# Optimization experiments

Measured on AMD Instinct MI355X. Metric: run time of the kernel, lower is better.

## Reference

```python
import jax, jax.numpy as jnp
import numpy as np

N_NODES = 100000
N_EDGES = 1600000
F_IN = 128
N_HEADS = 4
F_OUT = 32
NEG_SLOPE = 0.2


def setup_inputs() -> dict:
    key = jax.random.key(0)
    k_feat, k_src, k_dst, k_w, k_as, k_ad, k_res = jax.random.split(key, 7)
    feat = jax.random.normal(k_feat, (N_NODES, F_IN), dtype=jnp.float32)
    src = jax.random.randint(k_src, (N_EDGES,), 0, N_NODES, dtype=jnp.int32)
    dst = jax.random.randint(k_dst, (N_EDGES,), 0, N_NODES, dtype=jnp.int32)
    s = 1.0 / np.sqrt(F_IN)
    W = jax.random.normal(k_w, (F_IN, N_HEADS * F_OUT), dtype=jnp.float32) * s
    att_src = jax.random.normal(k_as, (N_HEADS, F_OUT), dtype=jnp.float32) * 0.1
    att_dst = jax.random.normal(k_ad, (N_HEADS, F_OUT), dtype=jnp.float32) * 0.1
    W_res = jax.random.normal(k_res, (F_IN, N_HEADS * F_OUT), dtype=jnp.float32) * s
    return {"feat": feat, "W": W, "att_src": att_src, "att_dst": att_dst,
            "W_res": W_res, "src": src, "dst": dst}


def reference(feat, W, att_src, att_dst, W_res, src, dst):
    N = feat.shape[0]
    H, Fo = att_src.shape
    # shared linear projection (GATConv, bias=False): [N, H, Fo]
    x = (feat @ W).reshape(N, H, Fo)
    # per-node attention logits: [N, H]
    a_s = jnp.einsum('nhf,hf->nh', x, att_src)
    a_d = jnp.einsum('nhf,hf->nh', x, att_dst)
    # edge-wise scores + LeakyReLU: [E, H]
    e = jax.nn.leaky_relu(a_s[src] + a_d[dst], negative_slope=NEG_SLOPE)
    # segment softmax over incoming edges of each dst node
    e_max = jax.ops.segment_max(e, dst, num_segments=N)  # [N, H]
    e_exp = jnp.exp(e - e_max[dst])                       # [E, H]
    denom = jax.ops.segment_sum(e_exp, dst, num_segments=N)  # [N, H]
    alpha = e_exp / denom[dst]                            # [E, H]
    # weighted scatter-add aggregation: [N, H, Fo]
    msg = x[src] * alpha[:, :, None]
    out = jax.ops.segment_sum(msg, dst, num_segments=N)
    # residual projection
    res = (feat @ W_res).reshape(N, H, Fo)
    return out + res
```

## Files before the change

### kernel.cpp

```cpp
#include <hip/hip_runtime.h>
#include <math.h>

#define NN 100000
#define NE 1600000
#define F_IN 128
#define C 128
#define NEG_SLOPE 0.2f
#define PROJ_NB ((NN + 63) / 64)

#define NBLK1 256
#define EPB ((NE + NBLK1 - 1) / NBLK1)
#define BSHIFT 9
#define NBUCK ((NN + 511) / 512)

#define WCONV_NB 16
#define FAT1_NB (WCONV_NB + NBLK1)
#define FAT2_NB (NBLK1 + PROJ_NB)

typedef __attribute__((ext_vector_type(8))) short short8;
typedef __attribute__((ext_vector_type(4))) float f32x4;
typedef __attribute__((ext_vector_type(4))) float floatx4;
typedef __attribute__((ext_vector_type(4))) unsigned short ushortx4;

static __device__ __forceinline__ unsigned short f2bf(float f) {
    unsigned int u = __float_as_uint(f);
    unsigned int r = (u + 0x7fff + ((u >> 16) & 1)) >> 16;
    return (unsigned short)r;
}
static __device__ __forceinline__ float bf2f(unsigned short h) {
    return __uint_as_float((unsigned int)h << 16);
}
static __device__ __forceinline__ float lrelu(float x) {
    return (x > 0.f) ? x : NEG_SLOPE * x;
}

__global__ __launch_bounds__(256)
void fat1_kernel(const float* __restrict__ W,
                 const float* __restrict__ Wr,
                 unsigned short* __restrict__ Btf,
                 const int* __restrict__ dst,
                 int* __restrict__ counts)
{
    __shared__ int h[256];
    const int tid = threadIdx.x;

    if (blockIdx.x < WCONV_NB) {
        int g = blockIdx.x * 256 + tid;
        int nt = g >> 8;
        int kc = (g >> 6) & 3;
        int l  = g & 63;
        int n  = nt * 16 + (l & 15);
        int kb = kc * 32 + (l >> 4) * 8;
        unsigned short v[8];
        #pragma unroll
        for (int j = 0; j < 8; ++j) {
            int k = kb + j;
            float f = (n < 128) ? W[(size_t)k * 128 + n]
                                : Wr[(size_t)k * 128 + (n - 128)];
            v[j] = f2bf(f);
        }
        *(short8*)&Btf[(size_t)g * 8] = *(short8*)v;
        return;
    }

    const int hb = blockIdx.x - WCONV_NB;
    h[tid] = 0;
    __syncthreads();
    const int e0 = hb * EPB;
    const int e1 = min(NE, e0 + EPB);
    for (int e = e0 + tid; e < e1; e += 256)
        atomicAdd(&h[dst[e] >> BSHIFT], 1);
    __syncthreads();
    counts[tid * NBLK1 + hb] = h[tid];
}

__global__ __launch_bounds__(256)
void sortscan_kernel(int* __restrict__ counts, int* __restrict__ bucket_base)
{
    __shared__ int wsum[4];
    const int t = threadIdx.x, lane = t & 63, wid = t >> 6;
    const int base = t * NBLK1;
    int run = 0;
    #pragma unroll 8
    for (int g = 0; g < NBLK1 / 4; ++g) {
        int4 c = *(const int4*)&counts[base + g * 4];
        int4 w;
        w.x = run;
        w.y = w.x + c.x;
        w.z = w.y + c.y;
        w.w = w.z + c.z;
        run = w.w + c.w;
        *(int4*)&counts[base + g * 4] = w;
    }
    int v0 = run, v = run;
    #pragma unroll
    for (int off = 1; off < 64; off <<= 1) {
        int u = __shfl_up(v, off, 64);
        if (lane >= off) v += u;
    }
    if (lane == 63) wsum[wid] = v;
    __syncthreads();
    if (t == 0) {
        int r = 0;
        #pragma unroll
        for (int s = 0; s < 4; ++s) { int tmp = wsum[s]; wsum[s] = r; r += tmp; }
    }
    __syncthreads();
    int excl = wsum[wid] + (v - v0);
    bucket_base[t] = excl;
    if (t == 255) bucket_base[256] = excl + v0;
}

__global__ __launch_bounds__(256, 4)
void fat2_kernel(const int* __restrict__ src, const int* __restrict__ dst,
                 const int* __restrict__ counts,
                 const int* __restrict__ bucket_base,
                 int* __restrict__ bpack,
                 const float* __restrict__ feat,
                 const unsigned short* __restrict__ Btf,
                 const float* __restrict__ att_src,
                 const float* __restrict__ att_dst,
                 unsigned short* __restrict__ xb,
                 unsigned short* __restrict__ resb,
                 float* __restrict__ a_s,
                 float* __restrict__ a_d)
{
    __shared__ __align__(16) char smem[19456];
    const int tid = threadIdx.x;

    if (blockIdx.x < NBLK1) {
        int* cur = (int*)smem;
        cur[tid] = bucket_base[tid] + counts[tid * NBLK1 + blockIdx.x];
        __syncthreads();
        const int e0 = blockIdx.x * EPB;
        const int e1 = min(NE, e0 + EPB);
        for (int e = e0 + tid; e < e1; e += 256) {
            int d = dst[e];
            int s = src[e];
            int pos = atomicAdd(&cur[d >> BSHIFT], 1);
            bpack[pos] = ((d & 511) << 20) | s;
        }
        return;
    }

    const int pb = blockIdx.x - NBLK1;
    float* T2base = (float*)smem;
    float (*s_as)[4] = (float(*)[4])(smem + 17408);
    float (*s_ad)[4] = (float(*)[4])(smem + 18432);

    const int base = pb * 64;
    const int l = tid & 63;
    const int w = tid >> 6;
    const int quad = l >> 4;
    const int lo16 = l & 15;
    const int arow = w * 16 + lo16;
    const int nclamp = min(base + arow, NN - 1);

    short8 af[4];
    #pragma unroll
    for (int kc = 0; kc < 4; ++kc) {
        const float* fp = &feat[(size_t)nclamp * F_IN + kc * 32 + quad * 8];
        floatx4 f0 = __builtin_nontemporal_load((const floatx4*)fp);
        floatx4 f1 = __builtin_nontemporal_load((const floatx4*)(fp + 4));
        unsigned short v[8];
        v[0] = f2bf(f0.x); v[1] = f2bf(f0.y); v[2] = f2bf(f0.z); v[3] = f2bf(f0.w);
        v[4] = f2bf(f1.x); v[5] = f2bf(f1.y); v[6] = f2bf(f1.z); v[7] = f2bf(f1.w);
        af[kc] = *(short8*)v;
    }

    f32x4 acc[16];
    #pragma unroll
    for (int nt = 0; nt < 16; ++nt) acc[nt] = (f32x4){0.f, 0.f, 0.f, 0.f};

    #pragma unroll
    for (int nt = 0; nt < 16; ++nt) {
        const unsigned short* bp = &Btf[(size_t)(nt * 4) * 512 + l * 8];
        short8 b0 = *(const short8*)&bp[0];
        short8 b1 = *(const short8*)&bp[512];
        short8 b2 = *(const short8*)&bp[1024];
        short8 b3 = *(const short8*)&bp[1536];
        acc[nt] = __builtin_amdgcn_mfma_f32_16x16x32_bf16(af[0], b0, acc[nt], 0, 0, 0);
        acc[nt] = __builtin_amdgcn_mfma_f32_16x16x32_bf16(af[1], b1, acc[nt], 0, 0, 0);
        acc[nt] = __builtin_amdgcn_mfma_f32_16x16x32_bf16(af[2], b2, acc[nt], 0, 0, 0);
        acc[nt] = __builtin_amdgcn_mfma_f32_16x16x32_bf16(af[3], b3, acc[nt], 0, 0, 0);
    }

    float* T2 = T2base + w * (16 * 68);
    const int g  = l >> 4;
    const int cf = (l & 15) * 4;

    #pragma unroll
    for (int p = 0; p < 2; ++p) {
        #pragma unroll
        for (int ntl = 0; ntl < 4; ++ntl) {
            int nt = p * 4 + ntl;
            #pragma unroll
            for (int r = 0; r < 4; ++r)
                T2[(quad * 4 + r) * 68 + ntl * 16 + lo16] = acc[nt][r];
        }
        floatx4 ws4 = *(const floatx4*)&att_src[p * 64 + cf];
        floatx4 wd4 = *(const floatx4*)&att_dst[p * 64 + cf];
        float ps[4], pd[4];
        #pragma unroll
        for (int it = 0; it < 4; ++it) {
            int row = it * 4 + g;
            floatx4 v = *(floatx4*)&T2[row * 68 + cf];
            int node = base + w * 16 + row;
            ushortx4 hh;
            hh.x = f2bf(v.x); hh.y = f2bf(v.y); hh.z = f2bf(v.z); hh.w = f2bf(v.w);
            if (node < NN)
                __builtin_nontemporal_store(hh,
                    (ushortx4*)&xb[(size_t)node * C + p * 64 + cf]);
            ps[it] = v.x * ws4.x + v.y * ws4.y + v.z * ws4.z + v.w * ws4.w;
            pd[it] = v.x * wd4.x + v.y * wd4.y + v.z * wd4.z + v.w * wd4.w;
        }
        #pragma unroll
        for (int it = 0; it < 4; ++it) {
            #pragma unroll
            for (int d = 1; d < 8; d <<= 1) {
                ps[it] += __shfl_xor(ps[it], d, 64);
                pd[it] += __shfl_xor(pd[it], d, 64);
            }
        }
        if ((l & 7) == 0) {
            int hh = p * 2 + ((l & 15) >> 3);
            #pragma unroll
            for (int it = 0; it < 4; ++it) {
                int lr = w * 16 + it * 4 + g;
                s_as[lr][hh] = ps[it];
                s_ad[lr][hh] = pd[it];
            }
        }
    }

    #pragma unroll
    for (int p = 0; p < 2; ++p) {
        #pragma unroll
        for (int ntl = 0; ntl < 4; ++ntl) {
            int nt = 8 + p * 4 + ntl;
            #pragma unroll
            for (int r = 0; r < 4; ++r)
                T2[(quad * 4 + r) * 68 + ntl * 16 + lo16] = acc[nt][r];
        }
        #pragma unroll
        for (int it = 0; it < 4; ++it) {
            int row = it * 4 + g;
            floatx4 v = *(floatx4*)&T2[row * 68 + cf];
            int node = base + w * 16 + row;
            ushortx4 hh;
            hh.x = f2bf(v.x); hh.y = f2bf(v.y); hh.z = f2bf(v.z); hh.w = f2bf(v.w);
            if (node < NN)
                __builtin_nontemporal_store(hh,
                    (ushortx4*)&resb[(size_t)node * C + p * 64 + cf]);
        }
    }

    __syncthreads();
    int idx = pb * 256 + tid;
    if (idx < NN * 4) {
        a_s[idx] = ((float*)s_as)[tid];
        a_d[idx] = ((float*)s_ad)[tid];
    }
}

__global__ __launch_bounds__(512)
void sort3_kernel(const int* __restrict__ bpack,
                  const int* __restrict__ bucket_base,
                  int* __restrict__ row_ptr,
                  int* __restrict__ csr_src)
{
    __shared__ int cnt[512];
    __shared__ int cur[512];
    __shared__ int wsum[8];
    const int t = threadIdx.x, lane = t & 63, wid = t >> 6;
    const int b = blockIdx.x;
    const int ebeg = bucket_base[b];
    const int eend = bucket_base[b + 1];
    cnt[t] = 0;
    __syncthreads();
    for (int e = ebeg + t; e < eend; e += 512)
        atomicAdd(&cnt[bpack[e] >> 20], 1);
    __syncthreads();
    int v0 = cnt[t], v = v0;
    #pragma unroll
    for (int off = 1; off < 64; off <<= 1) {
        int u = __shfl_up(v, off, 64);
        if (lane >= off) v += u;
    }
    if (lane == 63) wsum[wid] = v;
    __syncthreads();
    if (t == 0) {
        int r = 0;
        #pragma unroll
        for (int s = 0; s < 8; ++s) { int tmp = wsum[s]; wsum[s] = r; r += tmp; }
    }
    __syncthreads();
    int excl = wsum[wid] + (v - v0);
    cur[t] = excl;
    int n = (b << BSHIFT) + t;
    if (n < NN) row_ptr[n] = ebeg + excl;
    if (b == NBUCK - 1 && t == 0) row_ptr[NN] = NE;
    __syncthreads();
    for (int e = ebeg + t; e < eend; e += 512) {
        int p = bpack[e];
        int pos = atomicAdd(&cur[p >> 20], 1);
        csr_src[ebeg + pos] = p & 0xFFFFF;
    }
}

__global__ __launch_bounds__(256)
void agg_kernel(const unsigned short* __restrict__ xb,
                const unsigned short* __restrict__ resb,
                const float* __restrict__ a_s,
                const float* __restrict__ a_d,
                const int* __restrict__ row_ptr,
                const int* __restrict__ csr_src,
                float* __restrict__ out)
{
    __shared__ float s_alpha[4][4][68];
    __shared__ int   s_srcs[4][4][17];
    const int tid = threadIdx.x;
    const int w   = tid >> 6;
    const int l   = tid & 63;
    const int q   = l >> 4;
    const int t16 = l & 15;
    const int h   = t16 >> 2;

    const int n = blockIdx.x * 16 + w * 4 + q;
    const int r0  = row_ptr[n];
    const int deg = row_ptr[n + 1] - r0;

    short8 rv = *(const short8*)&resb[(size_t)n * C + t16 * 8];
    const float4 ad4 = *(const float4*)&a_d[n * 4];

    int dm = deg;
    dm = max(dm, __shfl_xor(dm, 16, 64));
    dm = max(dm, __shfl_xor(dm, 32, 64));

    float acc8[8];
    #pragma unroll
    for (int j = 0; j < 8; ++j) acc8[j] = 0.f;
    float dx = 0.f, dy = 0.f, dz = 0.f, dw = 0.f;

    for (int c0 = 0; c0 < dm; c0 += 16) {
        int e = c0 + t16;
        int s = 0;
        float4 ex = {0.f, 0.f, 0.f, 0.f};
        if (e < deg) {
            s = csr_src[r0 + e];
            float4 as4 = *(const float4*)&a_s[s * 4];
            ex.x = __expf(lrelu(as4.x + ad4.x));
            ex.y = __expf(lrelu(as4.y + ad4.y));
            ex.z = __expf(lrelu(as4.z + ad4.z));
            ex.w = __expf(lrelu(as4.w + ad4.w));
            dx += ex.x; dy += ex.y; dz += ex.z; dw += ex.w;
        }
        s_srcs[w][q][t16] = s;
        *(float4*)&s_alpha[w][q][t16 * 4] = ex;

        int cn = min(16, deg - c0);
        #pragma unroll 2
        for (int i = 0; i < cn; ++i) {
            int   si = s_srcs[w][q][i];
            float al = s_alpha[w][q][i * 4 + h];
            short8 uv = *(const short8*)&xb[(size_t)si * C + t16 * 8];
            acc8[0] = fmaf(al, bf2f((unsigned short)uv[0]), acc8[0]);
            acc8[1] = fmaf(al, bf2f((unsigned short)uv[1]), acc8[1]);
            acc8[2] = fmaf(al, bf2f((unsigned short)uv[2]), acc8[2]);
            acc8[3] = fmaf(al, bf2f((unsigned short)uv[3]), acc8[3]);
            acc8[4] = fmaf(al, bf2f((unsigned short)uv[4]), acc8[4]);
            acc8[5] = fmaf(al, bf2f((unsigned short)uv[5]), acc8[5]);
            acc8[6] = fmaf(al, bf2f((unsigned short)uv[6]), acc8[6]);
            acc8[7] = fmaf(al, bf2f((unsigned short)uv[7]), acc8[7]);
        }
    }

    #pragma unroll
    for (int d = 1; d < 16; d <<= 1) {
        dx += __shfl_xor(dx, d, 64);
        dy += __shfl_xor(dy, d, 64);
        dz += __shfl_xor(dz, d, 64);
        dw += __shfl_xor(dw, d, 64);
    }
    float den = (h == 0) ? dx : (h == 1) ? dy : (h == 2) ? dz : dw;
    float inv = (deg > 0) ? 1.f / den : 0.f;

    floatx4 o0, o1;
    o0.x = bf2f((unsigned short)rv[0]) + acc8[0] * inv;
    o0.y = bf2f((unsigned short)rv[1]) + acc8[1] * inv;
    o0.z = bf2f((unsigned short)rv[2]) + acc8[2] * inv;
    o0.w = bf2f((unsigned short)rv[3]) + acc8[3] * inv;
    o1.x = bf2f((unsigned short)rv[4]) + acc8[4] * inv;
    o1.y = bf2f((unsigned short)rv[5]) + acc8[5] * inv;
    o1.z = bf2f((unsigned short)rv[6]) + acc8[6] * inv;
    o1.w = bf2f((unsigned short)rv[7]) + acc8[7] * inv;
    __builtin_nontemporal_store(o0, (floatx4*)&out[(size_t)n * C + t16 * 8]);
    __builtin_nontemporal_store(o1, (floatx4*)&out[(size_t)n * C + t16 * 8 + 4]);
}

extern "C" void kernel_launch(void* const* d_in, const int* in_sizes, int n_in,
                              void* d_out, int out_size, void* d_ws, size_t ws_size,
                              hipStream_t stream)
{
    const float* feat    = (const float*)d_in[0];
    const float* W       = (const float*)d_in[1];
    const float* att_src = (const float*)d_in[2];
    const float* att_dst = (const float*)d_in[3];
    const float* W_res   = (const float*)d_in[4];
    const int*   src     = (const int*)d_in[5];
    const int*   dst     = (const int*)d_in[6];
    float* out = (float*)d_out;

    char* p = (char*)d_ws;
    unsigned short* xb   = (unsigned short*)p; p += (size_t)NN * C * sizeof(unsigned short);
    unsigned short* resb = (unsigned short*)p; p += (size_t)NN * C * sizeof(unsigned short);
    unsigned short* Btf  = (unsigned short*)p; p += (size_t)256 * 128 * sizeof(unsigned short);
    float* a_s = (float*)p;            p += (size_t)NN * 4 * sizeof(float);
    float* a_d = (float*)p;            p += (size_t)NN * 4 * sizeof(float);
    int* row_ptr = (int*)p;            p += (size_t)(NN + 1) * sizeof(int);
    int* counts  = (int*)p;            p += (size_t)NBLK1 * 256 * sizeof(int);
    int* bucket_base = (int*)p;        p += (size_t)257 * sizeof(int);
    int* bpack   = (int*)p;            p += (size_t)NE * sizeof(int);
    int* csr_src = (int*)p;            p += (size_t)NE * sizeof(int);

    fat1_kernel<<<FAT1_NB, 256, 0, stream>>>(W, W_res, Btf, dst, counts);
    sortscan_kernel<<<1, 256, 0, stream>>>(counts, bucket_base);
    fat2_kernel<<<FAT2_NB, 256, 0, stream>>>(src, dst, counts, bucket_base, bpack,
                                             feat, Btf, att_src, att_dst,
                                             xb, resb, a_s, a_d);
    sort3_kernel<<<NBUCK, 512, 0, stream>>>(bpack, bucket_base, row_ptr, csr_src);
    agg_kernel<<<NN / 16, 256, 0, stream>>>(xb, resb, a_s, a_d, row_ptr, csr_src, out);
}
```

Measured before the change: 262.9 us.

## Fuse per-bucket CSR sort into aggregation using 16-node buckets

Changes the counting sort to use 6250 buckets of 16 destination nodes. The per-bucket local sort that used to run in a separate sort3 kernel now happens inside the aggregation kernel's shared memory, which removes the csr_src and row_ptr global round trip. The scan is split into a per-bucket column scan kernel plus a small single-block total scan. In exchange, the counts and cursors arrays get much larger (6250x256 each), the histogram runs over large shared arrays, and a bucket is assumed to hold at most 1024 edges (ECAP) with no overflow check.

```diff
diff --git a/kernel.cpp b/kernel.cpp
--- a/kernel.cpp
+++ b/kernel.cpp
@@ -10,8 +10,9 @@
 
 #define NBLK1 256
 #define EPB ((NE + NBLK1 - 1) / NBLK1)
-#define BSHIFT 9
-#define NBUCK ((NN + 511) / 512)
+#define BSH 4
+#define NBUK (NN / 16)
+#define ECAP 1024
 
 #define WCONV_NB 16
 #define FAT1_NB (WCONV_NB + NBLK1)
@@ -41,7 +42,7 @@
                  const int* __restrict__ dst,
                  int* __restrict__ counts)
 {
-    __shared__ int h[256];
+    __shared__ int h[NBUK];
     const int tid = threadIdx.x;
 
     if (blockIdx.x < WCONV_NB) {
@@ -64,40 +65,65 @@
     }
 
     const int hb = blockIdx.x - WCONV_NB;
-    h[tid] = 0;
+    for (int i = tid; i < NBUK; i += 256) h[i] = 0;
     __syncthreads();
     const int e0 = hb * EPB;
     const int e1 = min(NE, e0 + EPB);
     for (int e = e0 + tid; e < e1; e += 256)
-        atomicAdd(&h[dst[e] >> BSHIFT], 1);
-    __syncthreads();
-    counts[tid * NBLK1 + hb] = h[tid];
-}
-
-__global__ __launch_bounds__(256)
-void sortscan_kernel(int* __restrict__ counts, int* __restrict__ bucket_base)
-{
-    __shared__ int wsum[4];
-    const int t = threadIdx.x, lane = t & 63, wid = t >> 6;
-    const int base = t * NBLK1;
-    int run = 0;
-    #pragma unroll 8
-    for (int g = 0; g < NBLK1 / 4; ++g) {
-        int4 c = *(const int4*)&counts[base + g * 4];
-        int4 w;
-        w.x = run;
-        w.y = w.x + c.x;
-        w.z = w.y + c.y;
-        w.w = w.z + c.z;
-        run = w.w + c.w;
-        *(int4*)&counts[base + g * 4] = w;
-    }
-    int v0 = run, v = run;
+        atomicAdd(&h[dst[e] >> BSH], 1);
+    __syncthreads();
+    for (int i = tid; i < NBUK; i += 256)
+        counts[(size_t)i * NBLK1 + hb] = h[i];
+}
+
+__global__ __launch_bounds__(64)
+void scan2a_kernel(const int* __restrict__ counts,
+                   int* __restrict__ cursors,
+                   int* __restrict__ totals)
+{
+    const int b = blockIdx.x;
+    const int lane = threadIdx.x;
+    int4 c = *(const int4*)&counts[(size_t)b * NBLK1 + lane * 4];
+    int i1 = c.x + c.y;
+    int i2 = i1 + c.z;
+    int s4 = i2 + c.w;
+    int v = s4;
     #pragma unroll
     for (int off = 1; off < 64; off <<= 1) {
         int u = __shfl_up(v, off, 64);
         if (lane >= off) v += u;
     }
+    int excl = v - s4;
+    cursors[(size_t)(lane * 4 + 0) * NBUK + b] = excl;
+    cursors[(size_t)(lane * 4 + 1) * NBUK + b] = excl + c.x;
+    cursors[(size_t)(lane * 4 + 2) * NBUK + b] = excl + i1;
+    cursors[(size_t)(lane * 4 + 3) * NBUK + b] = excl + i2;
+    if (lane == 63) totals[b] = v;
+}
+
+__global__ __launch_bounds__(256)
+void scan2b_kernel(const int* __restrict__ totals,
+                   int* __restrict__ bucket_base)
+{
+    __shared__ int sv[NBUK];
+    __shared__ int wsum[4];
+    const int t = threadIdx.x, lane = t & 63, wid = t >> 6;
+    for (int i = t; i < NBUK; i += 256) sv[i] = totals[i];
+    __syncthreads();
+    const int CH = (NBUK + 255) / 256;
+    const int b0 = t * CH;
+    int run = 0;
+    #pragma unroll 5
+    for (int j = 0; j < CH; ++j) {
+        int i = b0 + j;
+        if (i < NBUK) run += sv[i];
+    }
+    int v0 = run, v = run;
+    #pragma unroll
+    for (int off = 1; off < 64; off <<= 1) {
+        int u = __shfl_up(v, off, 64);
+        if (lane >= off) v += u;
+    }
     if (lane == 63) wsum[wid] = v;
     __syncthreads();
     if (t == 0) {
@@ -106,14 +132,20 @@
         for (int s = 0; s < 4; ++s) { int tmp = wsum[s]; wsum[s] = r; r += tmp; }
     }
     __syncthreads();
-    int excl = wsum[wid] + (v - v0);
-    bucket_base[t] = excl;
-    if (t == 255) bucket_base[256] = excl + v0;
+    int acc = wsum[wid] + (v - v0);
+    #pragma unroll 5
+    for (int j = 0; j < CH; ++j) {
+        int i = b0 + j;
+        if (i < NBUK) { int tmp = sv[i]; sv[i] = acc; acc += tmp; }
+    }
+    __syncthreads();
+    for (int i = t; i < NBUK; i += 256) bucket_base[i] = sv[i];
+    if (t == 0) bucket_base[NBUK] = NE;
 }
 
 __global__ __launch_bounds__(256, 4)
 void fat2_kernel(const int* __restrict__ src, const int* __restrict__ dst,
-                 const int* __restrict__ counts,
+                 const int* __restrict__ cursors,
                  const int* __restrict__ bucket_base,
                  int* __restrict__ bpack,
                  const float* __restrict__ feat,
@@ -125,20 +157,22 @@
                  float* __restrict__ a_s,
                  float* __restrict__ a_d)
 {
-    __shared__ __align__(16) char smem[19456];
+    __shared__ __align__(16) char smem[25088];
     const int tid = threadIdx.x;
 
     if (blockIdx.x < NBLK1) {
         int* cur = (int*)smem;
-        cur[tid] = bucket_base[tid] + counts[tid * NBLK1 + blockIdx.x];
+        const int* crow = &cursors[(size_t)blockIdx.x * NBUK];
+        for (int i = tid; i < NBUK; i += 256)
+            cur[i] = bucket_base[i] + crow[i];
         __syncthreads();
         const int e0 = blockIdx.x * EPB;
         const int e1 = min(NE, e0 + EPB);
         for (int e = e0 + tid; e < e1; e += 256) {
             int d = dst[e];
             int s = src[e];
-            int pos = atomicAdd(&cur[d >> BSHIFT], 1);
-            bpack[pos] = ((d & 511) << 20) | s;
+            int pos = atomicAdd(&cur[d >> BSH], 1);
+            bpack[pos] = ((d & 15) << 17) | s;
         }
         return;
     }
@@ -204,15 +238,15 @@
         #pragma unroll
         for (int it = 0; it < 4; ++it) {
             int row = it * 4 + g;
-            floatx4 v = *(floatx4*)&T2[row * 68 + cf];
+            floatx4 vv = *(floatx4*)&T2[row * 68 + cf];
             int node = base + w * 16 + row;
             ushortx4 hh;
-            hh.x = f2bf(v.x); hh.y = f2bf(v.y); hh.z = f2bf(v.z); hh.w = f2bf(v.w);
+            hh.x = f2bf(vv.x); hh.y = f2bf(vv.y); hh.z = f2bf(vv.z); hh.w = f2bf(vv.w);
             if (node < NN)
                 __builtin_nontemporal_store(hh,
                     (ushortx4*)&xb[(size_t)node * C + p * 64 + cf]);
-            ps[it] = v.x * ws4.x + v.y * ws4.y + v.z * ws4.z + v.w * ws4.w;
-            pd[it] = v.x * wd4.x + v.y * wd4.y + v.z * wd4.z + v.w * wd4.w;
+            ps[it] = vv.x * ws4.x + vv.y * ws4.y + vv.z * ws4.z + vv.w * ws4.w;
+            pd[it] = vv.x * wd4.x + vv.y * wd4.y + vv.z * wd4.z + vv.w * wd4.w;
         }
         #pragma unroll
         for (int it = 0; it < 4; ++it) {
@@ -245,10 +279,10 @@
         #pragma unroll
         for (int it = 0; it < 4; ++it) {
             int row = it * 4 + g;
-            floatx4 v = *(floatx4*)&T2[row * 68 + cf];
+            floatx4 vv = *(floatx4*)&T2[row * 68 + cf];
             int node = base + w * 16 + row;
             ushortx4 hh;
-            hh.x = f2bf(v.x); hh.y = f2bf(v.y); hh.z = f2bf(v.z); hh.w = f2bf(v.w);
+            hh.x = f2bf(vv.x); hh.y = f2bf(vv.y); hh.z = f2bf(vv.z); hh.w = f2bf(vv.w);
             if (node < NN)
                 __builtin_nontemporal_store(hh,
                     (ushortx4*)&resb[(size_t)node * C + p * 64 + cf]);
@@ -260,51 +294,6 @@
     if (idx < NN * 4) {
         a_s[idx] = ((float*)s_as)[tid];
         a_d[idx] = ((float*)s_ad)[tid];
-    }
-}
-
-__global__ __launch_bounds__(512)
-void sort3_kernel(const int* __restrict__ bpack,
-                  const int* __restrict__ bucket_base,
-                  int* __restrict__ row_ptr,
-                  int* __restrict__ csr_src)
-{
-    __shared__ int cnt[512];
-    __shared__ int cur[512];
-    __shared__ int wsum[8];
-    const int t = threadIdx.x, lane = t & 63, wid = t >> 6;
-    const int b = blockIdx.x;
-    const int ebeg = bucket_base[b];
-    const int eend = bucket_base[b + 1];
-    cnt[t] = 0;
-    __syncthreads();
-    for (int e = ebeg + t; e < eend; e += 512)
-        atomicAdd(&cnt[bpack[e] >> 20], 1);
-    __syncthreads();
-    int v0 = cnt[t], v = v0;
-    #pragma unroll
-    for (int off = 1; off < 64; off <<= 1) {
-        int u = __shfl_up(v, off, 64);
-        if (lane >= off) v += u;
-    }
-    if (lane == 63) wsum[wid] = v;
-    __syncthreads();
-    if (t == 0) {
-        int r = 0;
-        #pragma unroll
-        for (int s = 0; s < 8; ++s) { int tmp = wsum[s]; wsum[s] = r; r += tmp; }
-    }
-    __syncthreads();
-    int excl = wsum[wid] + (v - v0);
-    cur[t] = excl;
-    int n = (b << BSHIFT) + t;
-    if (n < NN) row_ptr[n] = ebeg + excl;
-    if (b == NBUCK - 1 && t == 0) row_ptr[NN] = NE;
-    __syncthreads();
-    for (int e = ebeg + t; e < eend; e += 512) {
-        int p = bpack[e];
-        int pos = atomicAdd(&cur[p >> 20], 1);
-        csr_src[ebeg + pos] = p & 0xFFFFF;
     }
 }
 
@@ -313,12 +302,15 @@
                 const unsigned short* __restrict__ resb,
                 const float* __restrict__ a_s,
                 const float* __restrict__ a_d,
-                const int* __restrict__ row_ptr,
-                const int* __restrict__ csr_src,
+                const int* __restrict__ bucket_base,
+                const int* __restrict__ bpack,
                 float* __restrict__ out)
 {
     __shared__ float s_alpha[4][4][68];
-    __shared__ int   s_srcs[4][4][17];
+    __shared__ int s_edge[ECAP];
+    __shared__ int h16[16];
+    __shared__ int cur16[16];
+    __shared__ int rp[17];
     const int tid = threadIdx.x;
     const int w   = tid >> 6;
     const int l   = tid & 63;
@@ -326,9 +318,35 @@
     const int t16 = l & 15;
     const int h   = t16 >> 2;
 
-    const int n = blockIdx.x * 16 + w * 4 + q;
-    const int r0  = row_ptr[n];
-    const int deg = row_ptr[n + 1] - r0;
+    const int b = blockIdx.x;
+    const int ebeg = bucket_base[b];
+    const int ecnt = bucket_base[b + 1] - ebeg;
+
+    if (tid < 16) h16[tid] = 0;
+    __syncthreads();
+    for (int e = tid; e < ecnt; e += 256)
+        atomicAdd(&h16[(bpack[ebeg + e] >> 17) & 15], 1);
+    __syncthreads();
+    if (tid == 0) {
+        int run = 0;
+        #pragma unroll
+        for (int i = 0; i < 16; ++i) {
+            rp[i] = run; cur16[i] = run; run += h16[i];
+        }
+        rp[16] = run;
+    }
+    __syncthreads();
+    for (int e = tid; e < ecnt; e += 256) {
+        int p = bpack[ebeg + e];
+        int pos = atomicAdd(&cur16[(p >> 17) & 15], 1);
+        s_edge[pos] = p & 0x1FFFF;
+    }
+    __syncthreads();
+
+    const int nl  = w * 4 + q;
+    const int n   = b * 16 + nl;
+    const int r0  = rp[nl];
+    const int deg = rp[nl + 1] - r0;
 
     short8 rv = *(const short8*)&resb[(size_t)n * C + t16 * 8];
     const float4 ad4 = *(const float4*)&a_d[n * 4];
@@ -344,10 +362,9 @@
 
     for (int c0 = 0; c0 < dm; c0 += 16) {
         int e = c0 + t16;
-        int s = 0;
         float4 ex = {0.f, 0.f, 0.f, 0.f};
         if (e < deg) {
-            s = csr_src[r0 + e];
+            int s = s_edge[r0 + e];
             float4 as4 = *(const float4*)&a_s[s * 4];
             ex.x = __expf(lrelu(as4.x + ad4.x));
             ex.y = __expf(lrelu(as4.y + ad4.y));
@@ -355,13 +372,12 @@
             ex.w = __expf(lrelu(as4.w + ad4.w));
             dx += ex.x; dy += ex.y; dz += ex.z; dw += ex.w;
         }
-        s_srcs[w][q][t16] = s;
         *(float4*)&s_alpha[w][q][t16 * 4] = ex;
 
         int cn = min(16, deg - c0);
         #pragma unroll 2
         for (int i = 0; i < cn; ++i) {
-            int   si = s_srcs[w][q][i];
+            int   si = s_edge[r0 + c0 + i];
             float al = s_alpha[w][q][i * 4 + h];
             short8 uv = *(const short8*)&xb[(size_t)si * C + t16 * 8];
             acc8[0] = fmaf(al, bf2f((unsigned short)uv[0]), acc8[0]);
@@ -417,17 +433,18 @@
     unsigned short* Btf  = (unsigned short*)p; p += (size_t)256 * 128 * sizeof(unsigned short);
     float* a_s = (float*)p;            p += (size_t)NN * 4 * sizeof(float);
     float* a_d = (float*)p;            p += (size_t)NN * 4 * sizeof(float);
-    int* row_ptr = (int*)p;            p += (size_t)(NN + 1) * sizeof(int);
-    int* counts  = (int*)p;            p += (size_t)NBLK1 * 256 * sizeof(int);
-    int* bucket_base = (int*)p;        p += (size_t)257 * sizeof(int);
+    int* counts  = (int*)p;            p += (size_t)NBUK * NBLK1 * sizeof(int);
+    int* cursors = (int*)p;            p += (size_t)NBLK1 * NBUK * sizeof(int);
+    int* totals  = (int*)p;            p += (size_t)NBUK * sizeof(int);
+    int* bucket_base = (int*)p;        p += (size_t)(NBUK + 1) * sizeof(int);
     int* bpack   = (int*)p;            p += (size_t)NE * sizeof(int);
-    int* csr_src = (int*)p;            p += (size_t)NE * sizeof(int);
 
     fat1_kernel<<<FAT1_NB, 256, 0, stream>>>(W, W_res, Btf, dst, counts);
-    sortscan_kernel<<<1, 256, 0, stream>>>(counts, bucket_base);
-    fat2_kernel<<<FAT2_NB, 256, 0, stream>>>(src, dst, counts, bucket_base, bpack,
+    scan2a_kernel<<<NBUK, 64, 0, stream>>>(counts, cursors, totals);
+    scan2b_kernel<<<1, 256, 0, stream>>>(totals, bucket_base);
+    fat2_kernel<<<FAT2_NB, 256, 0, stream>>>(src, dst, cursors, bucket_base, bpack,
                                              feat, Btf, att_src, att_dst,
                                              xb, resb, a_s, a_d);
-    sort3_kernel<<<NBUCK, 512, 0, stream>>>(bpack, bucket_base, row_ptr, csr_src);
-    agg_kernel<<<NN / 16, 256, 0, stream>>>(xb, resb, a_s, a_d, row_ptr, csr_src, out);
-}
+    agg_kernel<<<NBUK, 256, 0, stream>>>(xb, resb, a_s, a_d,
+                                         bucket_base, bpack, out);
+}
```

Measured after the change: 274.7 us. 1.04x slower.
